# Performance work log

Hardware: AMD Instinct MI355X
Metric: run time of the kernel (lower is better)

The kernel has to match this reference:

```python
import jax, jax.numpy as jnp
import numpy as np

DEPTH = 8  # remaining_depth at the root
N_INTERNAL = 2**DEPTH - 1  # 255, level-order indexed
N_LEAF = 2**DEPTH          # 256
CLAMP_MIN = 1e-5


def setup_inputs() -> dict:
    key = jax.random.key(0)
    k1, k2, k3 = jax.random.split(key, 3)
    B, D_in, D_out = 65536, 1024, 128
    x = jax.random.normal(k1, (B, D_in), dtype=jnp.float32)
    # one independent Linear(D_in,1) per internal node (deepcopy of split_function),
    # packed into a single [D_in, N_INTERNAL] matrix, level-order
    W_split = jax.random.normal(k2, (D_in, N_INTERNAL), dtype=jnp.float32) * (1.0 / np.sqrt(D_in))
    b_split = jnp.zeros((N_INTERNAL,), dtype=jnp.float32)
    # leaf values: uniform(-a, a) with a = sqrt(6/output_dim), per the torch init
    a = (6.0 / D_out) ** 0.5
    leaf_values = jax.random.uniform(k3, (N_LEAF, D_out), minval=-a, maxval=a, dtype=jnp.float32)
    return {"x": x, "W_split": W_split, "b_split": b_split, "leaf_values": leaf_values}


def reference(x, W_split, b_split, leaf_values):
    B = x.shape[0]
    # gate probability of every internal node in one batched GEMM: [B, N_INTERNAL]
    P = jax.nn.sigmoid(x @ W_split + b_split)
    # accumulate soft routing probability to each leaf, level by level
    probs = jnp.ones((B, 1), dtype=x.dtype)
    for d in range(DEPTH):
        p = P[:, 2**d - 1 : 2**(d + 1) - 1]  # gates at level d: [B, 2^d]
        # child order: left = (1-p), right = p (matches recursion ordering)
        probs = jnp.stack([(1.0 - p) * probs, p * probs], axis=-1).reshape(B, 2**(d + 1))
    out = probs @ leaf_values  # [B, D_out]: sum_leaf path_prob * value
    # regularization: sum over internal nodes of -0.5 * 2^-depth * mean_b log(clamp(p(1-p)))
    weights = jnp.concatenate(
        [jnp.full((2**d,), 2.0 ** (-d), dtype=x.dtype) for d in range(DEPTH)]
    )  # [N_INTERNAL]
    reg = jnp.sum(-0.5 * weights * jnp.mean(jnp.log(jnp.maximum(P * (1.0 - P), CLAMP_MIN)), axis=0))
    return out, reg
```

## Files before the change

### kernel.cpp

```cpp
#include <hip/hip_runtime.h>

#define B_TOT   65536
#define DIN     1024
#define NNODES  255
#define NPAD    256
#define DOUT    128
#define BM      64
#define BK      64

typedef __attribute__((ext_vector_type(8))) _Float16      f16x8;
typedef __attribute__((ext_vector_type(4))) float         f32x4;
typedef __attribute__((ext_vector_type(4))) unsigned short u16x4;
typedef __attribute__((ext_vector_type(8))) unsigned short u16x8;
typedef unsigned short u16;
typedef unsigned int   u32;

__device__ __forceinline__ u16 f2h(float f) {
  _Float16 h = (_Float16)f;
  return __builtin_bit_cast(u16, h);
}
__device__ __forceinline__ float h2f(u16 b) {
  return (float)__builtin_bit_cast(_Float16, b);
}

__device__ __forceinline__ int swz64(int row, int col) {
  return (row << 6) + ((((col >> 3) ^ row) & 7) << 3) + (col & 7);
}
__device__ __forceinline__ int swzP(int row, int col) {
  int g = col >> 3;
  int gs = (g & ~7) | ((g ^ row) & 7);
  return (row << 8) + (gs << 3) + (col & 7);
}

__global__ void prep_w(const float* __restrict__ Wsp, u16* __restrict__ Wt) {
  int t = blockIdx.x * 256 + threadIdx.x;
  int n = t & 255, k = t >> 8;
  float v = (n < NNODES) ? Wsp[k * NNODES + n] : 0.0f;
  Wt[n * DIN + k] = f2h(v);
}

__global__ void prep_leaf(const float* __restrict__ leaf, u16* __restrict__ lT) {
  int t = blockIdx.x * 256 + threadIdx.x;
  int j = t & 127, l = t >> 7;
  lT[j * NPAD + l] = f2h(leaf[l * DOUT + j]);
}

__global__ __launch_bounds__(256) void fused_sdt(
    const float* __restrict__ x, const float* __restrict__ bsp,
    const u16* __restrict__ Wt, const u16* __restrict__ lT,
    float* __restrict__ out, float* __restrict__ regp)
{
  __shared__ char smem[49184] __attribute__((aligned(16)));
  u16* xs  = (u16*)smem;
  u16* ws  = (u16*)(smem + 8192);
  u16* PB  = (u16*)smem;
  u16* lTs = (u16*)(smem + 32768);
  float* red = (float*)(smem + 49152);

  const int tid  = threadIdx.x;
  const int lane = tid & 63;
  const int w    = tid >> 6;
  const int l15  = lane & 15;
  const int quad = lane >> 4;
  const int blk  = blockIdx.x;

  const float* xg = x + (size_t)blk * BM * DIN;

  f32x4 acc[4][4];
  #pragma unroll
  for (int mt = 0; mt < 4; ++mt)
    #pragma unroll
    for (int nt = 0; nt < 4; ++nt) {
      f32x4 z = {0.0f, 0.0f, 0.0f, 0.0f};
      acc[mt][nt] = z;
    }

  for (int kc = 0; kc < DIN / BK; ++kc) {
    const int k0 = kc * BK;
    __syncthreads();
    #pragma unroll
    for (int i = 0; i < 4; ++i) {
      int idx = i * 256 + tid;
      int row = idx >> 4, kg = idx & 15;
      float4 v = *(const float4*)(xg + row * DIN + k0 + kg * 4);
      u16x4 h;
      h.x = f2h(v.x); h.y = f2h(v.y); h.z = f2h(v.z); h.w = f2h(v.w);
      *(u16x4*)&xs[swz64(row, kg * 4)] = h;
    }
    #pragma unroll
    for (int i = 0; i < 8; ++i) {
      int idx = i * 256 + tid;
      int n = idx >> 3, kg = idx & 7;
      u16x8 v = *(const u16x8*)(Wt + n * DIN + k0 + kg * 8);
      *(u16x8*)&ws[swz64(n, kg * 8)] = v;
    }
    __syncthreads();
    #pragma unroll
    for (int ks = 0; ks < 2; ++ks) {
      const int kk = ks * 32 + quad * 8;
      f16x8 A[4], Bf[4];
      #pragma unroll
      for (int mt = 0; mt < 4; ++mt)
        A[mt] = *(const f16x8*)&xs[swz64(mt * 16 + l15, kk)];
      #pragma unroll
      for (int nt = 0; nt < 4; ++nt)
        Bf[nt] = *(const f16x8*)&ws[swz64(w * 64 + nt * 16 + l15, kk)];
      #pragma unroll
      for (int mt = 0; mt < 4; ++mt)
        #pragma unroll
        for (int nt = 0; nt < 4; ++nt)
          acc[mt][nt] = __builtin_amdgcn_mfma_f32_16x16x32_f16(
              A[mt], Bf[nt], acc[mt][nt], 0, 0, 0);
    }
  }
  __syncthreads();

  float rsum = 0.0f;
  float bv[4];
  #pragma unroll
  for (int nt = 0; nt < 4; ++nt) {
    int c = w * 64 + nt * 16 + l15;
    bv[nt] = (c < NNODES) ? bsp[c] : 0.0f;
  }
  #pragma unroll
  for (int mt = 0; mt < 4; ++mt) {
    #pragma unroll
    for (int nt = 0; nt < 4; ++nt) {
      int c = w * 64 + nt * 16 + l15;
      #pragma unroll
      for (int r = 0; r < 4; ++r) {
        int row = mt * 16 + quad * 4 + r;
        float z = acc[mt][nt][r] + bv[nt];
        float e = __expf(-z);
        float p = __builtin_amdgcn_rcpf(1.0f + e);
        PB[swzP(row, c)] = f2h(p);
        if (c < NNODES) {
          float v = fmaxf(p * (1.0f - p), 1e-5f);
          int d = 31 - __clz(c + 1);
          float wgt = __builtin_bit_cast(float, (u32)(127 - d) << 23);
          rsum += wgt * __logf(v);
        }
      }
    }
  }
  #pragma unroll
  for (int off = 32; off > 0; off >>= 1) rsum += __shfl_down(rsum, off, 64);
  if (lane == 0) red[w] = rsum;
  __syncthreads();
  if (tid == 0) {
    float s = (red[0] + red[1] + red[2] + red[3]) * (-0.5f / 65536.0f);
    atomicAdd(regp, s);
  }

  for (int rr = 0; rr < 16; ++rr) {
    int row = (w << 4) + rr;
    float prod = 1.0f;
    #pragma unroll
    for (int d = 0; d < 6; ++d) {
      int node = (1 << d) - 1 + (lane >> (6 - d));
      float pv = h2f(PB[swzP(row, node)]);
      prod *= ((lane >> (5 - d)) & 1) ? pv : (1.0f - pv);
    }
    float p6  = h2f(PB[swzP(row, 63 + lane)]);
    float p7a = h2f(PB[swzP(row, 127 + 2 * lane)]);
    float p7b = h2f(PB[swzP(row, 128 + 2 * lane)]);
    float a0 = prod * (1.0f - p6), a1 = prod * p6;
    u16x4 o;
    o.x = f2h(a0 * (1.0f - p7a));
    o.y = f2h(a0 * p7a);
    o.z = f2h(a1 * (1.0f - p7b));
    o.w = f2h(a1 * p7b);
    *(u16x4*)&PB[swzP(row, 4 * lane)] = o;
  }

  f32x4 acc2[4][2];
  #pragma unroll
  for (int mt = 0; mt < 4; ++mt)
    #pragma unroll
    for (int nt = 0; nt < 2; ++nt) {
      f32x4 z = {0.0f, 0.0f, 0.0f, 0.0f};
      acc2[mt][nt] = z;
    }
  for (int kc = 0; kc < 4; ++kc) {
    __syncthreads();
    #pragma unroll
    for (int i = 0; i < 4; ++i) {
      int idx = i * 256 + tid;
      int j = idx >> 3, kg = idx & 7;
      u16x8 v = *(const u16x8*)(lT + j * NPAD + kc * 64 + kg * 8);
      *(u16x8*)&lTs[swz64(j, kg * 8)] = v;
    }
    __syncthreads();
    #pragma unroll
    for (int ks = 0; ks < 2; ++ks) {
      f16x8 Af[4], Bf2[2];
      #pragma unroll
      for (int mt = 0; mt < 4; ++mt)
        Af[mt] = *(const f16x8*)&PB[swzP(mt * 16 + l15, kc * 64 + ks * 32 + quad * 8)];
      #pragma unroll
      for (int nt = 0; nt < 2; ++nt)
        Bf2[nt] = *(const f16x8*)&lTs[swz64(w * 32 + nt * 16 + l15, ks * 32 + quad * 8)];
      #pragma unroll
      for (int mt = 0; mt < 4; ++mt)
        #pragma unroll
        for (int nt = 0; nt < 2; ++nt)
          acc2[mt][nt] = __builtin_amdgcn_mfma_f32_16x16x32_f16(
              Af[mt], Bf2[nt], acc2[mt][nt], 0, 0, 0);
    }
  }
  #pragma unroll
  for (int mt = 0; mt < 4; ++mt)
    #pragma unroll
    for (int nt = 0; nt < 2; ++nt)
      #pragma unroll
      for (int r = 0; r < 4; ++r) {
        int row = mt * 16 + quad * 4 + r;
        int col = w * 32 + nt * 16 + l15;
        out[(size_t)(blk * BM + row) * DOUT + col] = acc2[mt][nt][r];
      }
}

extern "C" void kernel_launch(void* const* d_in, const int* in_sizes, int n_in,
                              void* d_out, int out_size, void* d_ws, size_t ws_size,
                              hipStream_t stream) {
  (void)in_sizes; (void)n_in; (void)out_size; (void)ws_size;
  const float* x    = (const float*)d_in[0];
  const float* Wsp  = (const float*)d_in[1];
  const float* bsp  = (const float*)d_in[2];
  const float* leaf = (const float*)d_in[3];
  float* out  = (float*)d_out;
  float* regp = out + (size_t)B_TOT * DOUT;

  u16* Wt = (u16*)d_ws;
  u16* lT = Wt + NPAD * DIN;

  hipMemsetAsync(regp, 0, sizeof(float), stream);
  prep_w<<<(NPAD * DIN) / 256, 256, 0, stream>>>(Wsp, Wt);
  prep_leaf<<<(NPAD * DOUT) / 256, 256, 0, stream>>>(leaf, lT);
  fused_sdt<<<B_TOT / BM, 256, 0, stream>>>(x, bsp, Wt, lT, out, regp);
}
```

Baseline: 414.4 us.

## Register-prefetch next K tile during MFMA and tile-transpose the weight prep

The GEMM main loop now loads the next x and W K-tiles from global memory into registers while MFMAs run on the current tile, then writes them into shared memory after a barrier. This hides global load latency behind compute. The fp16 conversion uses packed cvt_pkrtz, which rounds toward zero, and launch bounds request 3 blocks per CU. The weight transpose prep kernel now uses a shared-memory tile so that both reads and writes are coalesced. The register prefetch buffers raise register pressure.

```diff
diff --git a/kernel.cpp b/kernel.cpp
--- a/kernel.cpp
+++ b/kernel.cpp
@@ -7,6 +7,7 @@
 #define DOUT    128
 #define BM      64
 #define BK      64
+#define NKT     (DIN / BK)
 
 typedef __attribute__((ext_vector_type(8))) _Float16      f16x8;
 typedef __attribute__((ext_vector_type(4))) float         f32x4;
@@ -22,6 +23,9 @@
 __device__ __forceinline__ float h2f(u16 b) {
   return (float)__builtin_bit_cast(_Float16, b);
 }
+__device__ __forceinline__ u32 pk2h(float a, float b) {
+  return __builtin_bit_cast(u32, __builtin_amdgcn_cvt_pkrtz(a, b));
+}
 
 __device__ __forceinline__ int swz64(int row, int col) {
   return (row << 6) + ((((col >> 3) ^ row) & 7) << 3) + (col & 7);
@@ -33,10 +37,28 @@
 }
 
 __global__ void prep_w(const float* __restrict__ Wsp, u16* __restrict__ Wt) {
-  int t = blockIdx.x * 256 + threadIdx.x;
-  int n = t & 255, k = t >> 8;
-  float v = (n < NNODES) ? Wsp[k * NNODES + n] : 0.0f;
-  Wt[n * DIN + k] = f2h(v);
+  __shared__ float t[64][65];
+  const int tid = threadIdx.x;
+  const int bn = blockIdx.x * 64;
+  const int bk = blockIdx.y * 64;
+  {
+    int n = tid & 63, kr0 = tid >> 6;
+    #pragma unroll
+    for (int i = 0; i < 16; ++i) {
+      int k = kr0 + i * 4;
+      int node = bn + n;
+      t[k][n] = (node < NNODES) ? Wsp[(size_t)(bk + k) * NNODES + node] : 0.0f;
+    }
+  }
+  __syncthreads();
+  {
+    int k = tid & 63, nr0 = tid >> 6;
+    #pragma unroll
+    for (int i = 0; i < 16; ++i) {
+      int node = nr0 + i * 4;
+      Wt[(size_t)(bn + node) * DIN + bk + k] = f2h(t[k][node]);
+    }
+  }
 }
 
 __global__ void prep_leaf(const float* __restrict__ leaf, u16* __restrict__ lT) {
@@ -45,7 +67,7 @@
   lT[j * NPAD + l] = f2h(leaf[l * DOUT + j]);
 }
 
-__global__ __launch_bounds__(256) void fused_sdt(
+__global__ __launch_bounds__(256, 3) void fused_sdt(
     const float* __restrict__ x, const float* __restrict__ bsp,
     const u16* __restrict__ Wt, const u16* __restrict__ lT,
     float* __restrict__ out, float* __restrict__ regp)
@@ -66,6 +88,14 @@
 
   const float* xg = x + (size_t)blk * BM * DIN;
 
+  const int xrow[4] = { (0*256 + tid) >> 4, (1*256 + tid) >> 4,
+                        (2*256 + tid) >> 4, (3*256 + tid) >> 4 };
+  const int xkg = tid & 15;
+  const int wn[8] = { (0*256 + tid) >> 3, (1*256 + tid) >> 3, (2*256 + tid) >> 3,
+                      (3*256 + tid) >> 3, (4*256 + tid) >> 3, (5*256 + tid) >> 3,
+                      (6*256 + tid) >> 3, (7*256 + tid) >> 3 };
+  const int wkg = tid & 7;
+
   f32x4 acc[4][4];
   #pragma unroll
   for (int mt = 0; mt < 4; ++mt)
@@ -75,26 +105,39 @@
       acc[mt][nt] = z;
     }
 
-  for (int kc = 0; kc < DIN / BK; ++kc) {
-    const int k0 = kc * BK;
-    __syncthreads();
-    #pragma unroll
-    for (int i = 0; i < 4; ++i) {
-      int idx = i * 256 + tid;
-      int row = idx >> 4, kg = idx & 15;
-      float4 v = *(const float4*)(xg + row * DIN + k0 + kg * 4);
-      u16x4 h;
-      h.x = f2h(v.x); h.y = f2h(v.y); h.z = f2h(v.z); h.w = f2h(v.w);
-      *(u16x4*)&xs[swz64(row, kg * 4)] = h;
-    }
-    #pragma unroll
-    for (int i = 0; i < 8; ++i) {
-      int idx = i * 256 + tid;
-      int n = idx >> 3, kg = idx & 7;
-      u16x8 v = *(const u16x8*)(Wt + n * DIN + k0 + kg * 8);
-      *(u16x8*)&ws[swz64(n, kg * 8)] = v;
-    }
-    __syncthreads();
+  float4 xp[4];
+  u16x8  wp[8];
+
+  #pragma unroll
+  for (int i = 0; i < 4; ++i)
+    xp[i] = *(const float4*)(xg + xrow[i] * DIN + xkg * 4);
+  #pragma unroll
+  for (int i = 0; i < 8; ++i)
+    wp[i] = *(const u16x8*)(Wt + wn[i] * DIN + wkg * 8);
+  #pragma unroll
+  for (int i = 0; i < 4; ++i) {
+    u32 lo = pk2h(xp[i].x, xp[i].y);
+    u32 hi = pk2h(xp[i].z, xp[i].w);
+    u16x4 h;
+    h.x = lo & 0xffff; h.y = lo >> 16;
+    h.z = hi & 0xffff; h.w = hi >> 16;
+    *(u16x4*)&xs[swz64(xrow[i], xkg * 4)] = h;
+  }
+  #pragma unroll
+  for (int i = 0; i < 8; ++i)
+    *(u16x8*)&ws[swz64(wn[i], wkg * 8)] = wp[i];
+
+  for (int kc = 0; kc < NKT; ++kc) {
+    __syncthreads();
+    if (kc + 1 < NKT) {
+      const int k1 = (kc + 1) * BK;
+      #pragma unroll
+      for (int i = 0; i < 4; ++i)
+        xp[i] = *(const float4*)(xg + xrow[i] * DIN + k1 + xkg * 4);
+      #pragma unroll
+      for (int i = 0; i < 8; ++i)
+        wp[i] = *(const u16x8*)(Wt + wn[i] * DIN + k1 + wkg * 8);
+    }
     #pragma unroll
     for (int ks = 0; ks < 2; ++ks) {
       const int kk = ks * 32 + quad * 8;
@@ -111,6 +154,21 @@
         for (int nt = 0; nt < 4; ++nt)
           acc[mt][nt] = __builtin_amdgcn_mfma_f32_16x16x32_f16(
               A[mt], Bf[nt], acc[mt][nt], 0, 0, 0);
+    }
+    __syncthreads();
+    if (kc + 1 < NKT) {
+      #pragma unroll
+      for (int i = 0; i < 4; ++i) {
+        u32 lo = pk2h(xp[i].x, xp[i].y);
+        u32 hi = pk2h(xp[i].z, xp[i].w);
+        u16x4 h;
+        h.x = lo & 0xffff; h.y = lo >> 16;
+        h.z = hi & 0xffff; h.w = hi >> 16;
+        *(u16x4*)&xs[swz64(xrow[i], xkg * 4)] = h;
+      }
+      #pragma unroll
+      for (int i = 0; i < 8; ++i)
+        *(u16x8*)&ws[swz64(wn[i], wkg * 8)] = wp[i];
     }
   }
   __syncthreads();
@@ -234,8 +292,8 @@
   u16* Wt = (u16*)d_ws;
   u16* lT = Wt + NPAD * DIN;
 
-  hipMemsetAsync(regp, 0, sizeof(float), stream);
-  prep_w<<<(NPAD * DIN) / 256, 256, 0, stream>>>(Wsp, Wt);
+  (void)hipMemsetAsync(regp, 0, sizeof(float), stream);
+  prep_w<<<dim3(4, 16), 256, 0, stream>>>(Wsp, Wt);
   prep_leaf<<<(NPAD * DOUT) / 256, 256, 0, stream>>>(leaf, lT);
   fused_sdt<<<B_TOT / BM, 256, 0, stream>>>(x, bsp, Wt, lT, out, regp);
 }
```

Result: slower. 426.5 us (+2.9%).

## Pre-swizzle W tiles and load via direct global-to-LDS, drop leaf LDS staging

Applied to the files above, without the earlier changes.

prep_w now transposes W through shared memory and writes it in k-chunk tiles already in the swizzled LDS layout. The main kernel can then copy each W tile straight into LDS with global_load_lds instead of going through registers. The leaf matrix is read directly from global (L2-resident) in the second GEMM, which removes its LDS staging and the per-chunk barriers and shrinks shared memory. This allows a launch bound of 3 blocks per CU. The x conversion uses packed cvt_pkrtz, which rounds toward zero and slightly changes numerics.

```diff
diff --git a/kernel.cpp b/kernel.cpp
--- a/kernel.cpp
+++ b/kernel.cpp
@@ -7,6 +7,7 @@
 #define DOUT    128
 #define BM      64
 #define BK      64
+#define NKT     (DIN / BK)
 
 typedef __attribute__((ext_vector_type(8))) _Float16      f16x8;
 typedef __attribute__((ext_vector_type(4))) float         f32x4;
@@ -22,6 +23,14 @@
 __device__ __forceinline__ float h2f(u16 b) {
   return (float)__builtin_bit_cast(_Float16, b);
 }
+__device__ __forceinline__ u32 pk2h(float a, float b) {
+  return __builtin_bit_cast(u32, __builtin_amdgcn_cvt_pkrtz(a, b));
+}
+__device__ __forceinline__ void cp16_g2s(const u16* g, u16* l) {
+  __builtin_amdgcn_global_load_lds(
+      (const __attribute__((address_space(1))) unsigned int*)g,
+      (__attribute__((address_space(3))) unsigned int*)l, 16, 0, 0);
+}
 
 __device__ __forceinline__ int swz64(int row, int col) {
   return (row << 6) + ((((col >> 3) ^ row) & 7) << 3) + (col & 7);
@@ -32,11 +41,30 @@
   return (row << 8) + (gs << 3) + (col & 7);
 }
 
-__global__ void prep_w(const float* __restrict__ Wsp, u16* __restrict__ Wt) {
-  int t = blockIdx.x * 256 + threadIdx.x;
-  int n = t & 255, k = t >> 8;
-  float v = (n < NNODES) ? Wsp[k * NNODES + n] : 0.0f;
-  Wt[n * DIN + k] = f2h(v);
+__global__ void prep_w(const float* __restrict__ Wsp, u16* __restrict__ WtT) {
+  __shared__ float t[64][65];
+  const int tid = threadIdx.x;
+  const int bn = blockIdx.x * 64;
+  const int kc = blockIdx.y;
+  const int bk = kc * 64;
+  {
+    int n = tid & 63, kr0 = tid >> 6;
+    #pragma unroll
+    for (int i = 0; i < 16; ++i) {
+      int k = kr0 + i * 4;
+      int node = bn + n;
+      t[k][n] = (node < NNODES) ? Wsp[(size_t)(bk + k) * NNODES + node] : 0.0f;
+    }
+  }
+  __syncthreads();
+  {
+    int k = tid & 63, nr0 = tid >> 6;
+    #pragma unroll
+    for (int i = 0; i < 16; ++i) {
+      int node = nr0 + i * 4;
+      WtT[kc * (NPAD * BK) + swz64(bn + node, k)] = f2h(t[k][node]);
+    }
+  }
 }
 
 __global__ void prep_leaf(const float* __restrict__ leaf, u16* __restrict__ lT) {
@@ -45,17 +73,16 @@
   lT[j * NPAD + l] = f2h(leaf[l * DOUT + j]);
 }
 
-__global__ __launch_bounds__(256) void fused_sdt(
+__global__ __launch_bounds__(256, 3) void fused_sdt(
     const float* __restrict__ x, const float* __restrict__ bsp,
-    const u16* __restrict__ Wt, const u16* __restrict__ lT,
+    const u16* __restrict__ WtT, const u16* __restrict__ lT,
     float* __restrict__ out, float* __restrict__ regp)
 {
-  __shared__ char smem[49184] __attribute__((aligned(16)));
+  __shared__ char smem[40960] __attribute__((aligned(16)));
   u16* xs  = (u16*)smem;
   u16* ws  = (u16*)(smem + 8192);
   u16* PB  = (u16*)smem;
-  u16* lTs = (u16*)(smem + 32768);
-  float* red = (float*)(smem + 49152);
+  float* red = (float*)(smem + 32768);
 
   const int tid  = threadIdx.x;
   const int lane = tid & 63;
@@ -75,24 +102,28 @@
       acc[mt][nt] = z;
     }
 
-  for (int kc = 0; kc < DIN / BK; ++kc) {
+  for (int kc = 0; kc < NKT; ++kc) {
     const int k0 = kc * BK;
     __syncthreads();
+    {
+      const u16* wtile = WtT + kc * (NPAD * BK);
+      #pragma unroll
+      for (int i = 0; i < 8; ++i) {
+        int chunk = w * 8 + i;
+        cp16_g2s(wtile + chunk * 512 + lane * 8, ws + chunk * 512);
+      }
+    }
     #pragma unroll
     for (int i = 0; i < 4; ++i) {
       int idx = i * 256 + tid;
       int row = idx >> 4, kg = idx & 15;
       float4 v = *(const float4*)(xg + row * DIN + k0 + kg * 4);
+      u32 lo = pk2h(v.x, v.y);
+      u32 hi = pk2h(v.z, v.w);
       u16x4 h;
-      h.x = f2h(v.x); h.y = f2h(v.y); h.z = f2h(v.z); h.w = f2h(v.w);
+      h.x = lo & 0xffff; h.y = lo >> 16;
+      h.z = hi & 0xffff; h.w = hi >> 16;
       *(u16x4*)&xs[swz64(row, kg * 4)] = h;
-    }
-    #pragma unroll
-    for (int i = 0; i < 8; ++i) {
-      int idx = i * 256 + tid;
-      int n = idx >> 3, kg = idx & 7;
-      u16x8 v = *(const u16x8*)(Wt + n * DIN + k0 + kg * 8);
-      *(u16x8*)&ws[swz64(n, kg * 8)] = v;
     }
     __syncthreads();
     #pragma unroll
@@ -172,6 +203,7 @@
     o.w = f2h(a1 * p7b);
     *(u16x4*)&PB[swzP(row, 4 * lane)] = o;
   }
+  __syncthreads();
 
   f32x4 acc2[4][2];
   #pragma unroll
@@ -182,24 +214,16 @@
       acc2[mt][nt] = z;
     }
   for (int kc = 0; kc < 4; ++kc) {
-    __syncthreads();
-    #pragma unroll
-    for (int i = 0; i < 4; ++i) {
-      int idx = i * 256 + tid;
-      int j = idx >> 3, kg = idx & 7;
-      u16x8 v = *(const u16x8*)(lT + j * NPAD + kc * 64 + kg * 8);
-      *(u16x8*)&lTs[swz64(j, kg * 8)] = v;
-    }
-    __syncthreads();
     #pragma unroll
     for (int ks = 0; ks < 2; ++ks) {
+      const int kk = kc * 64 + ks * 32 + quad * 8;
       f16x8 Af[4], Bf2[2];
       #pragma unroll
-      for (int mt = 0; mt < 4; ++mt)
-        Af[mt] = *(const f16x8*)&PB[swzP(mt * 16 + l15, kc * 64 + ks * 32 + quad * 8)];
-      #pragma unroll
       for (int nt = 0; nt < 2; ++nt)
-        Bf2[nt] = *(const f16x8*)&lTs[swz64(w * 32 + nt * 16 + l15, ks * 32 + quad * 8)];
+        Bf2[nt] = *(const f16x8*)&lT[(w * 32 + nt * 16 + l15) * NPAD + kk];
+      #pragma unroll
+      for (int mt = 0; mt < 4; ++mt)
+        Af[mt] = *(const f16x8*)&PB[swzP(mt * 16 + l15, kk)];
       #pragma unroll
       for (int mt = 0; mt < 4; ++mt)
         #pragma unroll
@@ -231,11 +255,11 @@
   float* out  = (float*)d_out;
   float* regp = out + (size_t)B_TOT * DOUT;
 
-  u16* Wt = (u16*)d_ws;
-  u16* lT = Wt + NPAD * DIN;
-
-  hipMemsetAsync(regp, 0, sizeof(float), stream);
-  prep_w<<<(NPAD * DIN) / 256, 256, 0, stream>>>(Wsp, Wt);
+  u16* WtT = (u16*)d_ws;
+  u16* lT  = WtT + NPAD * DIN;
+
+  (void)hipMemsetAsync(regp, 0, sizeof(float), stream);
+  prep_w<<<dim3(4, 16), 256, 0, stream>>>(Wsp, WtT);
   prep_leaf<<<(NPAD * DOUT) / 256, 256, 0, stream>>>(leaf, lT);
-  fused_sdt<<<B_TOT / BM, 256, 0, stream>>>(x, bsp, Wt, lT, out, regp);
-}
+  fused_sdt<<<B_TOT / BM, 256, 0, stream>>>(x, bsp, WtT, lT, out, regp);
+}
```

Result: no change. 409.1 us (-1.3%).
